# Kernel optimization log

Hardware: AMD Instinct MI355X
Metric: run time of the kernel (lower is better)

Reference implementation:

```python
import jax, jax.numpy as jnp
import numpy as np

HEADS = 8
HEAD_DIM = 64


def setup_inputs() -> dict:
    key = jax.random.key(0)
    ks = jax.random.split(key, 6)
    B, NQ, NC, D = 4, 1024, 8192, 512
    inner = HEADS * HEAD_DIM  # 512
    return {
        "x": jax.random.normal(ks[0], (B, NQ, D), dtype=jnp.float32),
        "context": jax.random.normal(ks[1], (B, NC, D), dtype=jnp.float32),
        "Wq": jax.random.normal(ks[2], (D, inner), dtype=jnp.float32) * (D ** -0.5),
        "Wkv": jax.random.normal(ks[3], (D, 2 * inner), dtype=jnp.float32) * (D ** -0.5),
        "Wout": jax.random.normal(ks[4], (inner, D), dtype=jnp.float32) * (inner ** -0.5),
        "bout": jax.random.normal(ks[5], (D,), dtype=jnp.float32) * 0.02,
    }


def reference(x, context, Wq, Wkv, Wout, bout):
    h, d = HEADS, HEAD_DIM
    scale = d ** -0.5
    b, nq, _ = x.shape
    nc = context.shape[1]
    q = x @ Wq                       # [b, nq, h*d]
    kv = context @ Wkv               # [b, nc, 2*h*d]
    k, v = jnp.split(kv, 2, axis=-1)
    # b n (h d) -> b h n d
    q = q.reshape(b, nq, h, d).transpose(0, 2, 1, 3)
    k = k.reshape(b, nc, h, d).transpose(0, 2, 1, 3)
    v = v.reshape(b, nc, h, d).transpose(0, 2, 1, 3)
    sim = jnp.einsum('bhid,bhjd->bhij', q, k) * scale  # [b, h, nq, nc]
    attn = jax.nn.softmax(sim, axis=-1)
    out = jnp.einsum('bhij,bhjd->bhid', attn, v)       # [b, h, nq, d]
    out = out.transpose(0, 2, 1, 3).reshape(b, nq, h * d)
    out = out @ Wout + bout          # [b, nq, queries_dim]
    return out.astype(x.dtype)
```

## Files before the change

kernel.cpp:

```cpp
#include <hip/hip_runtime.h>

#define B_   4
#define NQ_  1024
#define NC_  8192
#define D_   512
#define H_   8
#define HD_  64
#define NSPLIT 4
#define NCS  (NC_ / NSPLIT)

typedef __attribute__((ext_vector_type(4))) float f32x4;
typedef __attribute__((ext_vector_type(16))) float f32x16;
typedef __attribute__((ext_vector_type(8))) short s16x8;
typedef __attribute__((ext_vector_type(4))) unsigned short u16x4;

__device__ inline unsigned short f2bf(float f) {
  unsigned int u = __float_as_uint(f);
  u += 0x7fffu + ((u >> 16) & 1u);
  return (unsigned short)(u >> 16);
}

#define GLL16(g, l)                                                            \
  __builtin_amdgcn_global_load_lds(                                            \
      (const __attribute__((address_space(1))) void*)(g),                      \
      (__attribute__((address_space(3))) void*)(l), 16, 0, 0)

__global__ __launch_bounds__(256, 8)
void cvt_all(const float* __restrict__ x, const float* __restrict__ ctx,
             const float* __restrict__ Wq, const float* __restrict__ Wkv,
             const float* __restrict__ Wout,
             unsigned short* __restrict__ x_bf, unsigned short* __restrict__ ctx_bf,
             unsigned short* __restrict__ wqT, unsigned short* __restrict__ wkvT,
             unsigned short* __restrict__ woutT) {
  const int tid = blockIdx.x * 256 + threadIdx.x;
  const int stride = gridDim.x * 256;
  const int NCTX4 = 32768 * 512 / 4, NX4 = 4096 * 512 / 4;
  for (int i = tid; i < NCTX4 + NX4; i += stride) {
    const float4 v = (i < NCTX4) ? ((const float4*)ctx)[i]
                                 : ((const float4*)x)[i - NCTX4];
    u16x4 o;
    o.x = f2bf(v.x); o.y = f2bf(v.y); o.z = f2bf(v.z); o.w = f2bf(v.w);
    if (i < NCTX4) *(u16x4*)&ctx_bf[(long)i * 4] = o;
    else           *(u16x4*)&x_bf[(long)(i - NCTX4) * 4] = o;
  }
  const int NWQ = 512 * 512, NWKV = 512 * 1024;
  for (int i = tid; i < NWQ + NWKV + NWQ; i += stride) {
    if (i < NWQ) {
      int nn = i >> 9, kk = i & 511;
      wqT[i] = f2bf(Wq[kk * 512 + nn] * 0.18033688f);
    } else if (i < NWQ + NWKV) {
      int j = i - NWQ, nn = j >> 9, kk = j & 511;
      wkvT[j] = f2bf(Wkv[kk * 1024 + nn]);
    } else {
      int j = i - NWQ - NWKV, nn = j >> 9, kk = j & 511;
      woutT[j] = f2bf(Wout[kk * 512 + nn]);
    }
  }
}

template <int BM, int MODE>
__global__ __launch_bounds__(256, BM == 128 ? 2 : 4)
void gemm_bt(const unsigned short* __restrict__ A,
             const unsigned short* __restrict__ BT,
             void* __restrict__ C, const float* __restrict__ bias,
             unsigned short* __restrict__ vt,
             int M, int N, int K) {
  constexpr int MR = BM / 32;
  constexpr int SMEM = (MODE == 2) ? (128 * 72) : (BM * 64);
  __shared__ unsigned short smem[SMEM < BM * 64 ? BM * 64 : SMEM];
  unsigned short* As = smem;
  unsigned short* Bs = smem + BM * 32;
  const int tid = threadIdx.x;
  const int wid = tid >> 6;
  const int lane = tid & 63;
  const int l15 = lane & 15, l4 = lane >> 4;
  const int wr = wid >> 1, wc = wid & 1;
  const long brow = (long)blockIdx.y * BM;
  const long bcol = (long)blockIdx.x * BM;
  f32x4 acc[MR][MR] = {};

  for (int k0 = 0; k0 < K; k0 += 32) {
#pragma unroll
    for (int i = 0; i < BM / 64; ++i) {
      int c = i * 256 + tid;
      const unsigned short* ga = A  + (brow + (c >> 2)) * (long)K + k0 + (c & 3) * 8;
      const unsigned short* gb = BT + (bcol + (c >> 2)) * (long)K + k0 + (c & 3) * 8;
      GLL16(ga, (char*)As + i * 4096 + wid * 1024);
      GLL16(gb, (char*)Bs + i * 4096 + wid * 1024);
    }
    __syncthreads();
    s16x8 af[MR], bf[MR];
#pragma unroll
    for (int mi = 0; mi < MR; ++mi)
      af[mi] = *(const s16x8*)&As[(wr * (BM / 2) + mi * 16 + l15) * 32 + l4 * 8];
#pragma unroll
    for (int ni = 0; ni < MR; ++ni)
      bf[ni] = *(const s16x8*)&Bs[(wc * (BM / 2) + ni * 16 + l15) * 32 + l4 * 8];
#pragma unroll
    for (int mi = 0; mi < MR; ++mi)
#pragma unroll
      for (int ni = 0; ni < MR; ++ni)
        acc[mi][ni] = __builtin_amdgcn_mfma_f32_16x16x32_bf16(
            af[mi], bf[ni], acc[mi][ni], 0, 0, 0);
    __syncthreads();
  }

  if (MODE == 2 && bcol >= 512) {
    unsigned short* T = smem;
#pragma unroll
    for (int p = 0; p < 2; ++p) {
      __syncthreads();
      if (wr == p) {
#pragma unroll
        for (int ni = 0; ni < MR; ++ni)
#pragma unroll
          for (int mi = 0; mi < MR; ++mi)
#pragma unroll
            for (int r = 0; r < 4; ++r)
              T[(wc * 64 + ni * 16 + l15) * 72 + mi * 16 + l4 * 4 + r] =
                  f2bf(acc[mi][ni][r]);
      }
      __syncthreads();
      int hd = tid >> 1, part = tid & 1;
      const unsigned short* src = &T[hd * 72 + part * 32];
      s16x8 v0 = *(const s16x8*)(src);
      s16x8 v1 = *(const s16x8*)(src + 8);
      s16x8 v2 = *(const s16x8*)(src + 16);
      s16x8 v3 = *(const s16x8*)(src + 24);
      int hdg = (int)(bcol - 512) + hd;
      int bb = (int)(brow >> 13);
      long vrow = (long)(bb * 8 + (hdg >> 6)) * 64 + (hdg & 63);
      long nc = (brow & (NC_ - 1)) + p * 64 + part * 32;
      unsigned short* dst = vt + vrow * NC_ + nc;
      *(s16x8*)(dst) = v0;      *(s16x8*)(dst + 8) = v1;
      *(s16x8*)(dst + 16) = v2; *(s16x8*)(dst + 24) = v3;
    }
    return;
  }

#pragma unroll
  for (int ni = 0; ni < MR; ++ni) {
    const long col = bcol + wc * (BM / 2) + ni * 16 + l15;
    float bv = 0.f;
    if (MODE == 1) bv = bias[col];
#pragma unroll
    for (int mi = 0; mi < MR; ++mi) {
      const long row0 = brow + wr * (BM / 2) + mi * 16 + l4 * 4;
#pragma unroll
      for (int r = 0; r < 4; ++r) {
        const long row = row0 + r;
        float v = acc[mi][ni][r];
        if (MODE == 1) ((float*)C)[row * N + col] = v + bv;
        else if (MODE == 0) ((unsigned short*)C)[row * N + col] = f2bf(v);
        else ((unsigned short*)C)[row * 512 + col] = f2bf(v);
      }
    }
  }
}

__global__ __launch_bounds__(256, 2)
void attn_fwd(const unsigned short* __restrict__ q,
              const unsigned short* __restrict__ kq,
              const unsigned short* __restrict__ vt,
              float* __restrict__ Op, float* __restrict__ lp) {
  __shared__ char smem[33792];
  unsigned short* Ks = (unsigned short*)smem;
  unsigned short* Vs = (unsigned short*)(smem + 16384);
  float* red  = (float*)smem;
  float* lred = (float*)(smem + 32768);

  const int tid = threadIdx.x;
  const int wid = tid >> 6;
  const int lane = tid & 63;
  const int l31 = lane & 31, l5 = lane >> 5;
  const int id = blockIdx.x;
  const int g  = ((id >> 3) >> 4) * 8 + (id & 7);
  const int qt = (id >> 3) & 15;
  const int bh = g & 31, z = g >> 5;
  const int b = bh >> 3, h = bh & 7;
  const int q0 = qt * 64;
  const int wkv = wid * 32;

  s16x8 qf[2][4];
#pragma unroll
  for (int qb = 0; qb < 2; ++qb)
#pragma unroll
    for (int dblk = 0; dblk < 4; ++dblk)
      qf[qb][dblk] = *(const s16x8*)&q[((long)(b * NQ_ + q0 + qb * 32 + l31)) * 512 +
                                       h * 64 + dblk * 16 + l5 * 8];

  f32x16 o[2][2] = {};
  float lrun[2] = {0.f, 0.f};

  for (int it = 0; it < NCS / 128; ++it) {
    const int nc0 = z * NCS + it * 128;
#pragma unroll
    for (int i = 0; i < 4; ++i) {
      int c = i * 256 + tid;
      int krow = c >> 3;
      int kcolb = ((c & 7) * 16) ^ ((krow & 7) << 4);
      const unsigned short* gk =
          kq + ((long)(b * NC_ + nc0 + krow)) * 512 + h * 64 + (kcolb >> 1);
      GLL16(gk, (char*)Ks + i * 4096 + wid * 1024);
      int vrow = c >> 4;
      int vcolb = ((c & 15) * 16) ^ ((vrow & 15) << 4);
      const unsigned short* gv =
          vt + ((long)(bh * 64 + vrow)) * NC_ + nc0 + (vcolb >> 1);
      GLL16(gv, (char*)Vs + i * 4096 + wid * 1024);
    }
    __syncthreads();

    f32x16 st[2] = {};
    const int krow = wkv + l31;
#pragma unroll
    for (int dblk = 0; dblk < 4; ++dblk) {
      s16x8 kf = *(const s16x8*)((const char*)Ks + krow * 128 +
                                 ((dblk * 32 + l5 * 16) ^ ((krow & 7) << 4)));
#pragma unroll
      for (int qb = 0; qb < 2; ++qb)
        st[qb] = __builtin_amdgcn_mfma_f32_32x32x16_bf16(kf, qf[qb][dblk], st[qb], 0, 0, 0);
    }

    int pk[2][8];
#pragma unroll
    for (int qb = 0; qb < 2; ++qb) {
      float ps = 0.f;
#pragma unroll
      for (int r = 0; r < 16; ++r) {
        float v = __builtin_amdgcn_exp2f(st[qb][r]);
        st[qb][r] = v;
        ps += v;
      }
      lrun[qb] += ps;
#pragma unroll
      for (int w2 = 0; w2 < 8; ++w2)
        asm("v_cvt_pk_bf16_f32 %0, %1, %2"
            : "=v"(pk[qb][w2]) : "v"(st[qb][2 * w2]), "v"(st[qb][2 * w2 + 1]));
    }

#pragma unroll
    for (int kvb = 0; kvb < 2; ++kvb) {
      s16x8 vf[2];
#pragma unroll
      for (int dcb = 0; dcb < 2; ++dcb) {
        int drow = dcb * 32 + l31;
        vf[dcb] = *(const s16x8*)((const char*)Vs + drow * 256 +
                                  ((wkv * 2 + kvb * 32 + l5 * 16) ^ ((drow & 15) << 4)));
      }
#pragma unroll
      for (int qb = 0; qb < 2; ++qb) {
        int x1 = pk[qb][4 * kvb],     y1 = pk[qb][4 * kvb + 2];
        int x2 = pk[qb][4 * kvb + 1], y2 = pk[qb][4 * kvb + 3];
        asm("v_permlane32_swap_b32 %0, %1" : "+v"(x1), "+v"(y1));
        asm("v_permlane32_swap_b32 %0, %1" : "+v"(x2), "+v"(y2));
        int pw[4] = {x1, x2, y1, y2};
        s16x8 pa;
        __builtin_memcpy(&pa, pw, 16);
#pragma unroll
        for (int dcb = 0; dcb < 2; ++dcb)
          o[qb][dcb] = __builtin_amdgcn_mfma_f32_32x32x16_bf16(pa, vf[dcb], o[qb][dcb], 0, 0, 0);
      }
    }
    __syncthreads();
  }

  lrun[0] += __shfl_xor(lrun[0], 32, 64);
  lrun[1] += __shfl_xor(lrun[1], 32, 64);
  if (l5 == 0) {
    lred[wid * 64 + l31]      = lrun[0];
    lred[wid * 64 + 32 + l31] = lrun[1];
  }

#define O_IDX(qb, r) (qb * 32 + (r & 3) + ((r >> 2) << 3) + (l5 << 2))
  if (wid & 1) {
    float* dst = red + (wid >> 1) * 4096;
#pragma unroll
    for (int qb = 0; qb < 2; ++qb)
#pragma unroll
      for (int dcb = 0; dcb < 2; ++dcb)
#pragma unroll
        for (int r = 0; r < 16; ++r)
          dst[O_IDX(qb, r) * 64 + dcb * 32 + l31] = o[qb][dcb][r];
  }
  __syncthreads();
  if (!(wid & 1)) {
    const float* src = red + (wid >> 1) * 4096;
#pragma unroll
    for (int qb = 0; qb < 2; ++qb)
#pragma unroll
      for (int dcb = 0; dcb < 2; ++dcb)
#pragma unroll
        for (int r = 0; r < 16; ++r)
          o[qb][dcb][r] += src[O_IDX(qb, r) * 64 + dcb * 32 + l31];
  }
  __syncthreads();
  if (wid == 2) {
#pragma unroll
    for (int qb = 0; qb < 2; ++qb)
#pragma unroll
      for (int dcb = 0; dcb < 2; ++dcb)
#pragma unroll
        for (int r = 0; r < 16; ++r)
          red[O_IDX(qb, r) * 64 + dcb * 32 + l31] = o[qb][dcb][r];
  }
  __syncthreads();
  if (wid == 0) {
    const long obase = ((long)(z * 32 + bh)) * 1024 + q0;
#pragma unroll
    for (int qb = 0; qb < 2; ++qb)
#pragma unroll
      for (int dcb = 0; dcb < 2; ++dcb)
#pragma unroll
        for (int r = 0; r < 16; ++r) {
          int qrow = O_IDX(qb, r);
          float v = o[qb][dcb][r] + red[qrow * 64 + dcb * 32 + l31];
          Op[(obase + qrow) * 64 + dcb * 32 + l31] = v;
        }
    float ls = lred[lane] + lred[64 + lane] + lred[128 + lane] + lred[192 + lane];
    lp[obase + lane] = ls;
  }
#undef O_IDX
}

__global__ __launch_bounds__(256, 8)
void attn_combine(const float* __restrict__ Op, const float* __restrict__ lp,
                  unsigned short* __restrict__ att) {
  int idx = blockIdx.x * 256 + threadIdx.x;
  int col4 = idx & 127;
  int row = idx >> 7;
  int b = row >> 10, nq = row & 1023;
  int h = col4 >> 4, d4 = col4 & 15;
  float4 acc = {0.f, 0.f, 0.f, 0.f};
  float lsum = 0.f;
#pragma unroll
  for (int s = 0; s < NSPLIT; ++s) {
    const float4 v = *(const float4*)&Op[(((long)(s * 32 + b * 8 + h)) * 1024 + nq) * 64 + d4 * 4];
    acc.x += v.x; acc.y += v.y; acc.z += v.z; acc.w += v.w;
    lsum += lp[((long)(s * 32 + b * 8 + h)) * 1024 + nq];
  }
  float inv = 1.f / lsum;
  u16x4 o;
  o.x = f2bf(acc.x * inv); o.y = f2bf(acc.y * inv);
  o.z = f2bf(acc.z * inv); o.w = f2bf(acc.w * inv);
  *(u16x4*)&att[(long)row * 512 + col4 * 4] = o;
}

extern "C" void kernel_launch(void* const* d_in, const int* in_sizes, int n_in,
                              void* d_out, int out_size, void* d_ws, size_t ws_size,
                              hipStream_t stream) {
  (void)in_sizes; (void)n_in; (void)out_size; (void)ws_size;
  const float* x    = (const float*)d_in[0];
  const float* ctx  = (const float*)d_in[1];
  const float* Wq   = (const float*)d_in[2];
  const float* Wkv  = (const float*)d_in[3];
  const float* Wout = (const float*)d_in[4];
  const float* bout = (const float*)d_in[5];
  float* out = (float*)d_out;

  char* w = (char*)d_ws;
  unsigned short* x_bf   = (unsigned short*)w; w += (size_t)4096 * 512 * 2;
  unsigned short* ctx_bf = (unsigned short*)w; w += (size_t)32768 * 512 * 2;
  unsigned short* wqT    = (unsigned short*)w; w += (size_t)512 * 512 * 2;
  unsigned short* wkvT   = (unsigned short*)w; w += (size_t)1024 * 512 * 2;
  unsigned short* woutT  = (unsigned short*)w; w += (size_t)512 * 512 * 2;
  unsigned short* q_bf   = (unsigned short*)w; w += (size_t)4096 * 512 * 2;
  unsigned short* k_bf   = (unsigned short*)w; w += (size_t)32768 * 512 * 2;
  unsigned short* vt_bf  = (unsigned short*)w; w += (size_t)32 * 64 * NC_ * 2;
  unsigned short* att_bf = (unsigned short*)w; w += (size_t)4096 * 512 * 2;
  float* Opart = (float*)ctx_bf;
  float* lpart = (float*)x_bf;

  cvt_all<<<2048, 256, 0, stream>>>(x, ctx, Wq, Wkv, Wout,
                                    x_bf, ctx_bf, wqT, wkvT, woutT);

  gemm_bt<64, 0><<<dim3(8, 64), 256, 0, stream>>>(
      x_bf, wqT, q_bf, nullptr, nullptr, 4096, 512, 512);
  gemm_bt<128, 2><<<dim3(8, 256), 256, 0, stream>>>(
      ctx_bf, wkvT, k_bf, nullptr, vt_bf, 32768, 1024, 512);
  attn_fwd<<<2048, 256, 0, stream>>>(q_bf, k_bf, vt_bf, Opart, lpart);
  attn_combine<<<2048, 256, 0, stream>>>(Opart, lpart, att_bf);
  gemm_bt<64, 1><<<dim3(8, 64), 256, 0, stream>>>(
      att_bf, woutT, out, bout, nullptr, 4096, 512, 512);
}
```

Measured before the change: 296.0 us.

## Pre-pack K and V into MFMA fragment layout and load directly to registers

The KV projection GEMM now writes K and V in a packed per-(batch,head) layout that matches the MFMA operand fragments, so each lane reads its 16-byte fragment with a contiguous coalesced global load. The attention kernel drops the LDS staging of K/V tiles and the per-iteration barriers, with each wave loading its own 32-key chunk straight into registers. This removes LDS traffic and synchronisation, but there is no longer any sharing between waves, and global load latency is exposed without explicit prefetching. The K-side epilogue now uses scattered scalar stores.

```diff
diff --git a/kernel.cpp b/kernel.cpp
--- a/kernel.cpp
+++ b/kernel.cpp
@@ -129,11 +129,17 @@
       s16x8 v3 = *(const s16x8*)(src + 24);
       int hdg = (int)(bcol - 512) + hd;
       int bb = (int)(brow >> 13);
-      long vrow = (long)(bb * 8 + (hdg >> 6)) * 64 + (hdg & 63);
-      long nc = (brow & (NC_ - 1)) + p * 64 + part * 32;
-      unsigned short* dst = vt + vrow * NC_ + nc;
-      *(s16x8*)(dst) = v0;      *(s16x8*)(dst + 8) = v1;
-      *(s16x8*)(dst + 16) = v2; *(s16x8*)(dst + 24) = v3;
+      int hh = hdg >> 6, dh = hdg & 63;
+      int bh2 = bb * 8 + hh;
+      int ncb = (int)(brow & (NC_ - 1)) + p * 64 + part * 32;
+      int c = ncb >> 5;
+      int dcb = dh >> 5, l31v = dh & 31;
+      unsigned short* dst =
+          vt + (((long)(bh2 * 256 + c) * 2 + dcb) * 2) * 512 + l31v * 8;
+      *(s16x8*)(dst)       = v0;
+      *(s16x8*)(dst + 256) = v1;
+      *(s16x8*)(dst + 512) = v2;
+      *(s16x8*)(dst + 768) = v3;
     }
     return;
   }
@@ -152,7 +158,13 @@
         float v = acc[mi][ni][r];
         if (MODE == 1) ((float*)C)[row * N + col] = v + bv;
         else if (MODE == 0) ((unsigned short*)C)[row * N + col] = f2bf(v);
-        else ((unsigned short*)C)[row * 512 + col] = f2bf(v);
+        else {
+          int bb = (int)(row >> 13), nc = (int)(row & (NC_ - 1));
+          int hh = (int)col >> 6, dh = (int)col & 63;
+          long idx = ((long)((bb * 8 + hh) * 256 + (nc >> 5)) * 4 + (dh >> 4)) * 512 +
+                     ((dh >> 3) & 1) * 256 + (nc & 31) * 8 + (dh & 7);
+          ((unsigned short*)C)[idx] = f2bf(v);
+        }
       }
     }
   }
@@ -160,14 +172,11 @@
 
 __global__ __launch_bounds__(256, 2)
 void attn_fwd(const unsigned short* __restrict__ q,
-              const unsigned short* __restrict__ kq,
-              const unsigned short* __restrict__ vt,
+              const unsigned short* __restrict__ kp,
+              const unsigned short* __restrict__ vp,
               float* __restrict__ Op, float* __restrict__ lp) {
-  __shared__ char smem[33792];
-  unsigned short* Ks = (unsigned short*)smem;
-  unsigned short* Vs = (unsigned short*)(smem + 16384);
-  float* red  = (float*)smem;
-  float* lred = (float*)(smem + 32768);
+  __shared__ float red[8192];
+  __shared__ float lred[256];
 
   const int tid = threadIdx.x;
   const int wid = tid >> 6;
@@ -179,7 +188,6 @@
   const int bh = g & 31, z = g >> 5;
   const int b = bh >> 3, h = bh & 7;
   const int q0 = qt * 64;
-  const int wkv = wid * 32;
 
   s16x8 qf[2][4];
 #pragma unroll
@@ -192,34 +200,29 @@
   f32x16 o[2][2] = {};
   float lrun[2] = {0.f, 0.f};
 
+  const unsigned short* kbase = kp + (long)bh * 256 * 2048 + lane * 8;
+  const unsigned short* vbase = vp + (long)bh * 256 * 2048 + lane * 8;
+
   for (int it = 0; it < NCS / 128; ++it) {
-    const int nc0 = z * NCS + it * 128;
-#pragma unroll
-    for (int i = 0; i < 4; ++i) {
-      int c = i * 256 + tid;
-      int krow = c >> 3;
-      int kcolb = ((c & 7) * 16) ^ ((krow & 7) << 4);
-      const unsigned short* gk =
-          kq + ((long)(b * NC_ + nc0 + krow)) * 512 + h * 64 + (kcolb >> 1);
-      GLL16(gk, (char*)Ks + i * 4096 + wid * 1024);
-      int vrow = c >> 4;
-      int vcolb = ((c & 15) * 16) ^ ((vrow & 15) << 4);
-      const unsigned short* gv =
-          vt + ((long)(bh * 64 + vrow)) * NC_ + nc0 + (vcolb >> 1);
-      GLL16(gv, (char*)Vs + i * 4096 + wid * 1024);
-    }
-    __syncthreads();
+    const int c = z * 64 + it * 4 + wid;
+    const unsigned short* kc = kbase + (long)c * 2048;
+    const unsigned short* vc = vbase + (long)c * 2048;
+    s16x8 kf[4], vf[2][2];
+#pragma unroll
+    for (int dblk = 0; dblk < 4; ++dblk)
+      kf[dblk] = *(const s16x8*)(kc + dblk * 512);
+#pragma unroll
+    for (int dcb = 0; dcb < 2; ++dcb)
+#pragma unroll
+      for (int kvb = 0; kvb < 2; ++kvb)
+        vf[dcb][kvb] = *(const s16x8*)(vc + (dcb * 2 + kvb) * 512);
 
     f32x16 st[2] = {};
-    const int krow = wkv + l31;
-#pragma unroll
-    for (int dblk = 0; dblk < 4; ++dblk) {
-      s16x8 kf = *(const s16x8*)((const char*)Ks + krow * 128 +
-                                 ((dblk * 32 + l5 * 16) ^ ((krow & 7) << 4)));
+#pragma unroll
+    for (int dblk = 0; dblk < 4; ++dblk)
 #pragma unroll
       for (int qb = 0; qb < 2; ++qb)
-        st[qb] = __builtin_amdgcn_mfma_f32_32x32x16_bf16(kf, qf[qb][dblk], st[qb], 0, 0, 0);
-    }
+        st[qb] = __builtin_amdgcn_mfma_f32_32x32x16_bf16(kf[dblk], qf[qb][dblk], st[qb], 0, 0, 0);
 
     int pk[2][8];
 #pragma unroll
@@ -240,13 +243,6 @@
 
 #pragma unroll
     for (int kvb = 0; kvb < 2; ++kvb) {
-      s16x8 vf[2];
-#pragma unroll
-      for (int dcb = 0; dcb < 2; ++dcb) {
-        int drow = dcb * 32 + l31;
-        vf[dcb] = *(const s16x8*)((const char*)Vs + drow * 256 +
-                                  ((wkv * 2 + kvb * 32 + l5 * 16) ^ ((drow & 15) << 4)));
-      }
 #pragma unroll
       for (int qb = 0; qb < 2; ++qb) {
         int x1 = pk[qb][4 * kvb],     y1 = pk[qb][4 * kvb + 2];
@@ -258,10 +254,9 @@
         __builtin_memcpy(&pa, pw, 16);
 #pragma unroll
         for (int dcb = 0; dcb < 2; ++dcb)
-          o[qb][dcb] = __builtin_amdgcn_mfma_f32_32x32x16_bf16(pa, vf[dcb], o[qb][dcb], 0, 0, 0);
+          o[qb][dcb] = __builtin_amdgcn_mfma_f32_32x32x16_bf16(pa, vf[dcb][kvb], o[qb][dcb], 0, 0, 0);
       }
     }
-    __syncthreads();
   }
 
   lrun[0] += __shfl_xor(lrun[0], 32, 64);
@@ -364,8 +359,8 @@
   unsigned short* wkvT   = (unsigned short*)w; w += (size_t)1024 * 512 * 2;
   unsigned short* woutT  = (unsigned short*)w; w += (size_t)512 * 512 * 2;
   unsigned short* q_bf   = (unsigned short*)w; w += (size_t)4096 * 512 * 2;
-  unsigned short* k_bf   = (unsigned short*)w; w += (size_t)32768 * 512 * 2;
-  unsigned short* vt_bf  = (unsigned short*)w; w += (size_t)32 * 64 * NC_ * 2;
+  unsigned short* kp_bf  = (unsigned short*)w; w += (size_t)32768 * 512 * 2;
+  unsigned short* vp_bf  = (unsigned short*)w; w += (size_t)32 * 64 * NC_ * 2;
   unsigned short* att_bf = (unsigned short*)w; w += (size_t)4096 * 512 * 2;
   float* Opart = (float*)ctx_bf;
   float* lpart = (float*)x_bf;
@@ -376,8 +371,8 @@
   gemm_bt<64, 0><<<dim3(8, 64), 256, 0, stream>>>(
       x_bf, wqT, q_bf, nullptr, nullptr, 4096, 512, 512);
   gemm_bt<128, 2><<<dim3(8, 256), 256, 0, stream>>>(
-      ctx_bf, wkvT, k_bf, nullptr, vt_bf, 32768, 1024, 512);
-  attn_fwd<<<2048, 256, 0, stream>>>(q_bf, k_bf, vt_bf, Opart, lpart);
+      ctx_bf, wkvT, kp_bf, nullptr, vp_bf, 32768, 1024, 512);
+  attn_fwd<<<2048, 256, 0, stream>>>(q_bf, kp_bf, vp_bf, Opart, lpart);
   attn_combine<<<2048, 256, 0, stream>>>(Opart, lpart, att_bf);
   gemm_bt<64, 1><<<dim3(8, 64), 256, 0, stream>>>(
       att_bf, woutT, out, bout, nullptr, 4096, 512, 512);
```

After: 295.0 us. Within noise of the previous version (-0.3%).
